# Kernel tuning notes

Hardware: AMD Instinct MI355X
Metric: run time of the kernel (lower is better)

## Reference

```python
import jax, jax.numpy as jnp
import numpy as np

B, S, D, H, L, V = 8, 512, 1024, 16, 12, 30145
FF = 4 * D
NL = 2  # n_langs
EPS = 1e-12


def _ln(x, g, b):
    m = jnp.mean(x, axis=-1, keepdims=True)
    v = jnp.var(x, axis=-1, keepdims=True)
    return (x - m) * jax.lax.rsqrt(v + EPS) * g + b


def setup_inputs() -> dict:
    key = jax.random.key(0)
    ks = iter(jax.random.split(key, 32))
    std, estd = 0.02, 0.02
    d = {
        "input_ids": jax.random.randint(next(ks), (B, S), 0, V),
        "langs": jax.random.randint(next(ks), (B, S), 0, NL),
        "attention_mask": jnp.ones((B, S), jnp.float32),
        "word_emb": jax.random.normal(next(ks), (V, D), jnp.float32) * estd,
        "pos_emb": jax.random.normal(next(ks), (S, D), jnp.float32) * estd,
        "lang_emb": jax.random.normal(next(ks), (NL, D), jnp.float32) * estd,
        "ln_emb_g": jnp.ones((D,), jnp.float32),
        "ln_emb_b": jnp.zeros((D,), jnp.float32),
        "Wq": jax.random.normal(next(ks), (L, D, D), jnp.float32) * std,
        "bq": jnp.zeros((L, D), jnp.float32),
        "Wk": jax.random.normal(next(ks), (L, D, D), jnp.float32) * std,
        "bk": jnp.zeros((L, D), jnp.float32),
        "Wv": jax.random.normal(next(ks), (L, D, D), jnp.float32) * std,
        "bv": jnp.zeros((L, D), jnp.float32),
        "Wo": jax.random.normal(next(ks), (L, D, D), jnp.float32) * std,
        "bo": jnp.zeros((L, D), jnp.float32),
        "ln1_g": jnp.ones((L, D), jnp.float32),
        "ln1_b": jnp.zeros((L, D), jnp.float32),
        "W1": jax.random.normal(next(ks), (L, D, FF), jnp.float32) * std,
        "b1": jnp.zeros((L, FF), jnp.float32),
        "W2": jax.random.normal(next(ks), (L, FF, D), jnp.float32) * std,
        "b2": jnp.zeros((L, D), jnp.float32),
        "ln2_g": jnp.ones((L, D), jnp.float32),
        "ln2_b": jnp.zeros((L, D), jnp.float32),
    }
    return d


def reference(input_ids, langs, attention_mask, word_emb, pos_emb, lang_emb,
              ln_emb_g, ln_emb_b, Wq, bq, Wk, bk, Wv, bv, Wo, bo,
              ln1_g, ln1_b, W1, b1, W2, b2, ln2_g, ln2_b):
    dh = D // H
    scale = 1.0 / np.sqrt(dh).astype(np.float32)
    # embeddings: word + position + language, then LayerNorm, then pad-mask
    x = word_emb[input_ids] + pos_emb[None, :, :] + lang_emb[langs]  # [B,S,D]
    x = _ln(x, ln_emb_g, ln_emb_b)
    fmask = attention_mask  # [B,S], 1=keep
    x = x * fmask[:, :, None]
    neg = (-1e30) * (1.0 - fmask)[:, None, None, :]  # [B,1,1,S] additive mask

    def layer(x, p):
        Wq_, bq_, Wk_, bk_, Wv_, bv_, Wo_, bo_, g1, gb1, W1_, b1_, W2_, b2_, g2, gb2 = p
        q = ((x @ Wq_ + bq_) * scale).reshape(B, S, H, dh)
        k = (x @ Wk_ + bk_).reshape(B, S, H, dh)
        v = (x @ Wv_ + bv_).reshape(B, S, H, dh)
        scores = jnp.einsum('bqhd,bkhd->bhqk', q, k) + neg
        w = jax.nn.softmax(scores, axis=-1)
        ctx = jnp.einsum('bhqk,bkhd->bqhd', w, v).reshape(B, S, D)
        x = _ln(x + ctx @ Wo_ + bo_, g1, gb1)
        h = jax.nn.gelu(x @ W1_ + b1_, approximate=False)  # erf gelu as in source
        x = _ln(x + h @ W2_ + b2_, g2, gb2)
        x = x * fmask[:, :, None]
        return x, None

    params = (Wq, bq, Wk, bk, Wv, bv, Wo, bo, ln1_g, ln1_b, W1, b1, W2, b2, ln2_g, ln2_b)
    x, _ = jax.lax.scan(layer, x, params)
    return x
```

## Files before the change

### kernel.cpp

```cpp
#include <hip/hip_runtime.h>
#include <math.h>

typedef float  f32x4  __attribute__((ext_vector_type(4)));
typedef __bf16 bf16x8 __attribute__((ext_vector_type(8)));
typedef __bf16 bf16x4 __attribute__((ext_vector_type(4)));

#define DEV __device__ __forceinline__

DEV f32x4 mfma16(bf16x8 a, bf16x8 b, f32x4 c) {
    return __builtin_amdgcn_mfma_f32_16x16x32_bf16(a, b, c, 0, 0, 0);
}

DEV void async16(const void* g, void* l) {
    __builtin_amdgcn_global_load_lds((const __attribute__((address_space(1))) void*)g,
                                     (__attribute__((address_space(3))) void*)l, 16, 0, 0);
}

constexpr int B_  = 8;
constexpr int S_  = 512;
constexpr int D_  = 1024;
constexpr int H_  = 16;
constexpr int FF_ = 4096;
constexpr int ROWS = B_ * S_;

__global__ __launch_bounds__(256)
void embed_ln_kernel(const int* __restrict__ ids, const int* __restrict__ lgs,
                     const float* __restrict__ fmask,
                     const float* __restrict__ wemb, const float* __restrict__ pemb,
                     const float* __restrict__ lemb,
                     const float* __restrict__ g, const float* __restrict__ bb,
                     float* __restrict__ xf, __bf16* __restrict__ xb)
{
    __shared__ float2 red[4];
    const int row = blockIdx.x;
    const int s   = row & (S_ - 1);
    const int t   = threadIdx.x;
    const int lane = t & 63, w = t >> 6;
    const int id = ids[row], lg = lgs[row];

    float4 wv = *(const float4*)(wemb + ((size_t)id << 10) + t * 4);
    float4 pv = *(const float4*)(pemb + ((size_t)s  << 10) + t * 4);
    float4 lv = *(const float4*)(lemb + ((size_t)lg << 10) + t * 4);
    float a[4] = { wv.x + pv.x + lv.x, wv.y + pv.y + lv.y,
                   wv.z + pv.z + lv.z, wv.w + pv.w + lv.w };

    float sm = a[0] + a[1] + a[2] + a[3];
    float sq = a[0]*a[0] + a[1]*a[1] + a[2]*a[2] + a[3]*a[3];
#pragma unroll
    for (int o = 32; o > 0; o >>= 1) { sm += __shfl_down(sm, o); sq += __shfl_down(sq, o); }
    if (lane == 0) red[w] = make_float2(sm, sq);
    __syncthreads();
    float ts = red[0].x + red[1].x + red[2].x + red[3].x;
    float tq = red[0].y + red[1].y + red[2].y + red[3].y;
    float mean = ts * (1.0f / D_);
    float var  = tq * (1.0f / D_) - mean * mean;
    float rs   = rsqrtf(var + 1e-12f);
    float fm   = fmask[row];

    float4 gv = *(const float4*)(g  + t * 4);
    float4 bv = *(const float4*)(bb + t * 4);
    float o0 = ((a[0]-mean)*rs*gv.x + bv.x) * fm;
    float o1 = ((a[1]-mean)*rs*gv.y + bv.y) * fm;
    float o2 = ((a[2]-mean)*rs*gv.z + bv.z) * fm;
    float o3 = ((a[3]-mean)*rs*gv.w + bv.w) * fm;
    *(float4*)(xf + ((size_t)row << 10) + t * 4) = make_float4(o0, o1, o2, o3);
    bf16x4 ob; ob[0] = (__bf16)o0; ob[1] = (__bf16)o1; ob[2] = (__bf16)o2; ob[3] = (__bf16)o3;
    *(bf16x4*)(xb + ((size_t)row << 10) + t * 4) = ob;
}

template<int NP>
__global__ __launch_bounds__(256)
void ln_resN_kernel(const float* __restrict__ xin, const float* __restrict__ y0,
                    const float* __restrict__ y1,
                    const float* __restrict__ g, const float* __restrict__ bb,
                    const float* __restrict__ fmask,
                    float* __restrict__ xf_out, __bf16* __restrict__ xb_out)
{
    constexpr size_t MN = (size_t)ROWS * D_;
    __shared__ float2 red[4];
    const int row = blockIdx.x;
    const int t   = threadIdx.x;
    const int lane = t & 63, w = t >> 6;
    const size_t base = ((size_t)row << 10) + t * 4;

    float4 xv = *(const float4*)(xin + base);
    float4 yv = *(const float4*)(y0 + base);
    float a[4] = { xv.x + yv.x, xv.y + yv.y, xv.z + yv.z, xv.w + yv.w };
    if (NP == 4) {
        float4 p1 = *(const float4*)(y0 + base + MN);
        float4 p2 = *(const float4*)(y1 + base);
        float4 p3 = *(const float4*)(y1 + base + MN);
        a[0] += p1.x + p2.x + p3.x; a[1] += p1.y + p2.y + p3.y;
        a[2] += p1.z + p2.z + p3.z; a[3] += p1.w + p2.w + p3.w;
    }

    float sm = a[0] + a[1] + a[2] + a[3];
    float sq = a[0]*a[0] + a[1]*a[1] + a[2]*a[2] + a[3]*a[3];
#pragma unroll
    for (int o = 32; o > 0; o >>= 1) { sm += __shfl_down(sm, o); sq += __shfl_down(sq, o); }
    if (lane == 0) red[w] = make_float2(sm, sq);
    __syncthreads();
    float ts = red[0].x + red[1].x + red[2].x + red[3].x;
    float tq = red[0].y + red[1].y + red[2].y + red[3].y;
    float mean = ts * (1.0f / D_);
    float var  = tq * (1.0f / D_) - mean * mean;
    float rs   = rsqrtf(var + 1e-12f);
    float fm   = fmask ? fmask[row] : 1.0f;

    float4 gv = *(const float4*)(g  + t * 4);
    float4 bv = *(const float4*)(bb + t * 4);
    float o0 = ((a[0]-mean)*rs*gv.x + bv.x) * fm;
    float o1 = ((a[1]-mean)*rs*gv.y + bv.y) * fm;
    float o2 = ((a[2]-mean)*rs*gv.z + bv.z) * fm;
    float o3 = ((a[3]-mean)*rs*gv.w + bv.w) * fm;
    *(float4*)(xf_out + base) = make_float4(o0, o1, o2, o3);
    bf16x4 ob; ob[0] = (__bf16)o0; ob[1] = (__bf16)o1; ob[2] = (__bf16)o2; ob[3] = (__bf16)o3;
    *(bf16x4*)(xb_out + base) = ob;
}

__global__ __launch_bounds__(256)
void conv_all_kernel(const float* __restrict__ Wq, const float* __restrict__ Wk,
                     const float* __restrict__ Wv, const float* __restrict__ Wo,
                     const float* __restrict__ W1, const float* __restrict__ W2,
                     __bf16* __restrict__ qkvT, __bf16* __restrict__ woT,
                     __bf16* __restrict__ w1T, __bf16* __restrict__ w2T)
{
    __shared__ __bf16 tile[64][66];
    const int id = blockIdx.x;
    const float* src; __bf16* dst; int K, N, t;
    if (id < 1024) {
        const int m = id >> 8; t = id & 255; K = 1024; N = 1024;
        src = (m == 0) ? Wq : (m == 1) ? Wk : (m == 2) ? Wv : Wo;
        dst = (m == 3) ? woT : qkvT + (size_t)m * 1024 * 1024;
    } else if (id < 2048) {
        t = id - 1024; K = 1024; N = 4096; src = W1; dst = w1T;
    } else {
        t = id - 2048; K = 4096; N = 1024; src = W2; dst = w2T;
    }
    const int ktiles = K >> 6;
    const int tk = t % ktiles, tn = t / ktiles;
    const int k0 = tk << 6, n0 = tn << 6;
    const int tt = threadIdx.x;
#pragma unroll
    for (int i = 0; i < 16; ++i) {
        int idx = i * 256 + tt;
        int r = idx >> 6, c = idx & 63;
        tile[c][r] = (__bf16)src[(size_t)(k0 + r) * N + n0 + c];
    }
    __syncthreads();
#pragma unroll
    for (int i = 0; i < 16; ++i) {
        int idx = i * 256 + tt;
        int r = idx >> 6, c = idx & 63;
        dst[(size_t)(n0 + r) * K + k0 + c] = tile[r][c];
    }
}

template<int EPI>
__global__ __launch_bounds__(512, 2)
void gemm256_kernel(const __bf16* __restrict__ A, const __bf16* __restrict__ Bt,
                    const float* __restrict__ b0, const float* __restrict__ b1,
                    const float* __restrict__ b2,
                    __bf16* __restrict__ o0, __bf16* __restrict__ o1,
                    __bf16* __restrict__ o2,
                    float* __restrict__ oF0, float* __restrict__ oF1,
                    int M, int N, int K, int Kloc, int nTn, int tiles)
{
    __shared__ __bf16 lds[65536];
    const int tid  = threadIdx.x;
    const int lane = tid & 63;
    const int w    = tid >> 6;
    const int wr   = w >> 2, wc = w & 3;

    const int nwg = gridDim.x, bid = blockIdx.x;
    const int cpx = nwg >> 3;
    const int bswz = (bid & 7) * cpx + (bid >> 3);
    const int slice = bswz / tiles;
    const int tile  = bswz % tiles;
    const int bm = tile / nTn, bn = tile % nTn;
    const int m0 = bm << 8, n0 = bn << 8;
    const int ks = slice * Kloc;

    const int rrT = tid >> 3;
    const size_t swzK  = (size_t)(((tid & 7) ^ (rrT & 7)) * 8);
    const size_t aoff0 = (size_t)rrT * K + swzK;
    const size_t boff0 = (size_t)((rrT >> 5) * 64 + (rrT & 31)) * K + swzK;
    const size_t boff1 = (size_t)(((rrT >> 5) + 2) * 64 + (rrT & 31)) * K + swzK;
    const int wub = w * 512;

    const int aread = (wr * 64 + (lane & 15)) * 64;
    const int bread = (wc * 32 + (lane & 15)) * 64;
    const int csw0 = ((      (lane >> 4) * 16) ^ ((lane & 7) << 4)) >> 1;
    const int csw1 = ((64 +  (lane >> 4) * 16) ^ ((lane & 7) << 4)) >> 1;

    f32x4 acc[8][4] = {};
    bf16x8 a_[4][2], b_[2][2];

#define ST_A(p,h,kt) do {                                                     \
    const size_t gb = (size_t)(m0 + (h) * 64) * K + (kt);                     \
    async16(A + gb + aoff0,                  lds + ((p)*2+(h))*8192 + wub);   \
    async16(A + gb + (size_t)128*K + aoff0,  lds + ((p)*2+(h))*8192 + 4096 + wub); \
} while (0)
#define ST_B(p,h,kt) do {                                                     \
    const size_t gb = (size_t)(n0 + (h) * 32) * K + (kt);                     \
    async16(Bt + gb + boff0, lds + 32768 + ((p)*2+(h))*8192 + wub);           \
    async16(Bt + gb + boff1, lds + 32768 + ((p)*2+(h))*8192 + 4096 + wub);    \
} while (0)
#define DS_A(p,h) do {                                                        \
    const __bf16* base_ = lds + ((p)*2+(h))*8192 + aread;                     \
    _Pragma("unroll") for (int m_ = 0; m_ < 4; ++m_) {                        \
        a_[m_][0] = *(const bf16x8*)(base_ + m_*1024 + csw0);                 \
        a_[m_][1] = *(const bf16x8*)(base_ + m_*1024 + csw1);                 \
    }                                                                         \
} while (0)
#define DS_B(p,h) do {                                                        \
    const __bf16* base_ = lds + 32768 + ((p)*2+(h))*8192 + bread;             \
    _Pragma("unroll") for (int n_ = 0; n_ < 2; ++n_) {                        \
        b_[n_][0] = *(const bf16x8*)(base_ + n_*1024 + csw0);                 \
        b_[n_][1] = *(const bf16x8*)(base_ + n_*1024 + csw1);                 \
    }                                                                         \
} while (0)
#define MM(mb,nb) do {                                                        \
    _Pragma("unroll") for (int m_ = 0; m_ < 4; ++m_)                          \
    _Pragma("unroll") for (int n_ = 0; n_ < 2; ++n_)                          \
    _Pragma("unroll") for (int k_ = 0; k_ < 2; ++k_)                          \
        acc[(mb)+m_][(nb)+n_] = mfma16(a_[m_][k_], b_[n_][k_], acc[(mb)+m_][(nb)+n_]); \
} while (0)
#define SYNC do { __builtin_amdgcn_s_barrier();                               \
    asm volatile("s_waitcnt lgkmcnt(0)" ::: "memory");                        \
    __builtin_amdgcn_s_setprio(1); } while (0)
#define PEND do { __builtin_amdgcn_s_setprio(0);                              \
    __builtin_amdgcn_s_barrier(); } while (0)

    ST_A(0,0, ks);      ST_B(0,1, ks);      ST_A(0,1, ks);      ST_B(0,0, ks);
    ST_A(1,0, ks + 64); ST_B(1,1, ks + 64); ST_A(1,1, ks + 64);
    asm volatile("s_waitcnt vmcnt(6)" ::: "memory");
    __builtin_amdgcn_s_barrier();

    const int nIter = Kloc >> 7;
    for (int i = 0; i < nIter; ++i) {
        const bool nl = (i != nIter - 1);
        const int kt1 = ks + (2*i+1) * 64;
        const int kt2 = ks + (2*i+2) * 64;
        const int kt3 = kt2 + 64;
        DS_A(0,0); DS_B(0,0); ST_B(1,0,kt1);
        SYNC; MM(0,0); PEND;
        DS_B(0,1); if (nl) ST_A(0,0,kt2);
        SYNC; MM(0,2); PEND;
        DS_A(0,1); if (nl) ST_B(0,1,kt2);
        SYNC; MM(4,2); PEND;
        DS_B(0,0); if (nl) ST_A(0,1,kt2);
        SYNC; MM(4,0);
        __builtin_amdgcn_s_setprio(0);
        if (nl) asm volatile("s_waitcnt vmcnt(6)" ::: "memory");
        else    asm volatile("s_waitcnt vmcnt(0)" ::: "memory");
        __builtin_amdgcn_s_barrier();
        DS_A(1,0); DS_B(1,0); if (nl) ST_B(0,0,kt2);
        SYNC; MM(0,0); PEND;
        DS_B(1,1); if (nl) ST_A(1,0,kt3);
        SYNC; MM(0,2); PEND;
        DS_A(1,1); if (nl) ST_B(1,1,kt3);
        SYNC; MM(4,2); PEND;
        DS_B(1,0); if (nl) ST_A(1,1,kt3);
        SYNC; MM(4,0);
        __builtin_amdgcn_s_setprio(0);
        if (nl) asm volatile("s_waitcnt vmcnt(6)" ::: "memory");
        __builtin_amdgcn_s_barrier();
    }
#undef ST_A
#undef ST_B
#undef DS_A
#undef DS_B
#undef MM
#undef SYNC
#undef PEND

    const int mrow = m0 + wr * 128 + (lane >> 4) * 4;
    const int ncol = n0 + wc * 64 + (lane & 15);
    if (EPI == 0) {
        const int sel = n0 >> 10;
        __bf16* out = (sel == 0) ? o0 : (sel == 1) ? o1 : o2;
        const float* bp = (sel == 0) ? b0 : (sel == 1) ? b1 : b2;
        const float scl = (sel == 0) ? 0.125f : 1.0f;
        const int nc = ncol & 1023;
#pragma unroll
        for (int ni = 0; ni < 4; ++ni) {
            const float bvv = bp[nc + ni * 16];
#pragma unroll
            for (int mi = 0; mi < 8; ++mi)
#pragma unroll
                for (int r = 0; r < 4; ++r)
                    out[(size_t)(mrow + mi * 16 + r) * D_ + nc + ni * 16] =
                        (__bf16)((acc[mi][ni][r] + bvv) * scl);
        }
    } else if (EPI == 2) {
#pragma unroll
        for (int ni = 0; ni < 4; ++ni) {
            const float bvv = b0[ncol + ni * 16];
#pragma unroll
            for (int mi = 0; mi < 8; ++mi)
#pragma unroll
                for (int r = 0; r < 4; ++r) {
                    float v = acc[mi][ni][r] + bvv;
                    float ge = 0.5f * v * (1.0f + erff(v * 0.70710678118654752f));
                    o0[(size_t)(mrow + mi * 16 + r) * N + ncol + ni * 16] = (__bf16)ge;
                }
        }
    } else {
        const size_t MN = (size_t)M * N;
        float* Y = (slice < 2) ? (oF0 + (size_t)slice * MN) : (oF1 + (size_t)(slice - 2) * MN);
#pragma unroll
        for (int ni = 0; ni < 4; ++ni) {
            const float bvv = (slice == 0) ? b0[ncol + ni * 16] : 0.0f;
#pragma unroll
            for (int mi = 0; mi < 8; ++mi)
#pragma unroll
                for (int r = 0; r < 4; ++r)
                    Y[(size_t)(mrow + mi * 16 + r) * N + ncol + ni * 16] = acc[mi][ni][r] + bvv;
        }
    }
}

template<int EPI>
__global__ __launch_bounds__(256, 2)
void gemm_kernel(const __bf16* __restrict__ A, const __bf16* __restrict__ Bt,
                 const float* __restrict__ bias, float* __restrict__ Cf,
                 __bf16* __restrict__ Cb, int M, int N, int K, float scale)
{
    __shared__ __bf16 As[128 * 64];
    __shared__ __bf16 Bs[128 * 64];
    const int tid = threadIdx.x;
    const int lane = tid & 63;
    const int w = tid >> 6, wr = w >> 1, wc = w & 1;
    const int nT = N >> 7;
    const int nwg = gridDim.x;
    const int bid = blockIdx.x;
    const int cpx = nwg >> 3;
    const int bswz = (bid & 7) * cpx + (bid >> 3);
    const int bm = bswz / nT, bn = bswz % nT;
    const int m0 = bm << 7, n0 = bn << 7;

    f32x4 acc[4][4] = {};

    const int chr = tid >> 3, chc = tid & 7;
    const __bf16* ga = A  + (size_t)(m0 + chr) * K + chc * 8;
    const __bf16* gb = Bt + (size_t)(n0 + chr) * K + chc * 8;
    char* la = (char*)As + (tid & ~63) * 16;
    char* lb = (char*)Bs + (tid & ~63) * 16;

    const __bf16* arow = As + (wr * 64 + (lane & 15)) * 64 + (lane >> 4) * 8;
    const __bf16* brow = Bs + (wc * 64 + (lane & 15)) * 64 + (lane >> 4) * 8;

    for (int k0 = 0; k0 < K; k0 += 64) {
#pragma unroll
        for (int i = 0; i < 4; ++i) {
            async16(ga + (size_t)(i * 32) * K + k0, la + i * 4096);
            async16(gb + (size_t)(i * 32) * K + k0, lb + i * 4096);
        }
        __syncthreads();
#pragma unroll
        for (int kk = 0; kk < 2; ++kk) {
            bf16x8 af[4], bf[4];
#pragma unroll
            for (int i = 0; i < 4; ++i) af[i] = *(const bf16x8*)(arow + i * 16 * 64 + kk * 32);
#pragma unroll
            for (int i = 0; i < 4; ++i) bf[i] = *(const bf16x8*)(brow + i * 16 * 64 + kk * 32);
#pragma unroll
            for (int mi = 0; mi < 4; ++mi)
#pragma unroll
                for (int ni = 0; ni < 4; ++ni)
                    acc[mi][ni] = mfma16(af[mi], bf[ni], acc[mi][ni]);
        }
        __syncthreads();
    }

    const int mb = m0 + wr * 64 + ((lane >> 4) * 4);
    const int nb = n0 + wc * 64 + (lane & 15);
#pragma unroll
    for (int ni = 0; ni < 4; ++ni) {
        const float bvv = bias[nb + ni * 16];
#pragma unroll
        for (int mi = 0; mi < 4; ++mi)
#pragma unroll
            for (int r = 0; r < 4; ++r)
                Cf[(size_t)(mb + mi * 16 + r) * N + nb + ni * 16] =
                    (acc[mi][ni][r] + bvv) * scale;
    }
}

__global__ __launch_bounds__(256, 2)
void attn_kernel(const __bf16* __restrict__ q, const __bf16* __restrict__ k,
                 const __bf16* __restrict__ v, const float* __restrict__ fmask,
                 __bf16* __restrict__ ctx)
{
    __shared__ __bf16 Ks[256 * 64];
    __shared__ __bf16 Vt[64 * 264];
    __shared__ float  negm[S_];
    const int bid = blockIdx.x;
    const int qt = bid & 7, h = (bid >> 3) & 15, b = bid >> 7;
    const int tid = threadIdx.x, lane = tid & 63, w = tid >> 6;
    const int r7 = lane & 7;

    const __bf16* kbase = k + ((size_t)b * S_) * D_ + h * 64;
    const __bf16* vbase = v + ((size_t)b * S_) * D_ + h * 64;
    char* kl = (char*)Ks + (tid & ~63) * 16;
    const int srow  = tid >> 3;
    const int sslot = (tid & 7) ^ (srow & 7);

    for (int i = tid; i < S_; i += 256) negm[i] = (fmask[b * S_ + i] - 1.0f) * 1e30f;

    const __bf16* qbase = q + ((size_t)b * S_ + qt * 64 + w * 16) * D_ + h * 64;
    const bf16x8 qf0 = *(const bf16x8*)(qbase + (size_t)(lane & 15) * D_ + (lane >> 4) * 8);
    const bf16x8 qf1 = *(const bf16x8*)(qbase + (size_t)(lane & 15) * D_ + 32 + (lane >> 4) * 8);

    f32x4 sc[32];
#pragma unroll
    for (int i = 0; i < 32; ++i) { sc[i][0] = 0.f; sc[i][1] = 0.f; sc[i][2] = 0.f; sc[i][3] = 0.f; }

#pragma unroll
    for (int c = 0; c < 2; ++c) {
        if (c) __syncthreads();
#pragma unroll
        for (int i = 0; i < 8; ++i) {
            const int s = c * 256 + i * 32 + srow;
            async16(kbase + (size_t)s * D_ + sslot * 8, kl + i * 4096);
        }
        __syncthreads();
#pragma unroll
        for (int nf = 0; nf < 16; ++nf) {
            const __bf16* kr = Ks + (nf * 16 + (lane & 15)) * 64;
            const bf16x8 k0 = *(const bf16x8*)(kr + ((((lane >> 4))     ^ r7) << 3));
            const bf16x8 k1 = *(const bf16x8*)(kr + ((((lane >> 4) + 4) ^ r7) << 3));
            sc[c * 16 + nf] = mfma16(qf0, k0, sc[c * 16 + nf]);
            sc[c * 16 + nf] = mfma16(qf1, k1, sc[c * 16 + nf]);
        }
    }

    float mx[4] = { -3e38f, -3e38f, -3e38f, -3e38f };
#pragma unroll
    for (int i = 0; i < 32; ++i) {
        const int key = (i >> 4) * 256 + (i & 15) * 16 + (lane & 15);
        const float nm = negm[key];
#pragma unroll
        for (int r = 0; r < 4; ++r) { sc[i][r] += nm; mx[r] = fmaxf(mx[r], sc[i][r]); }
    }
#pragma unroll
    for (int o = 8; o > 0; o >>= 1)
#pragma unroll
        for (int r = 0; r < 4; ++r) mx[r] = fmaxf(mx[r], __shfl_xor(mx[r], o));
    float smr[4] = { 0.f, 0.f, 0.f, 0.f };
#pragma unroll
    for (int i = 0; i < 32; ++i)
#pragma unroll
        for (int r = 0; r < 4; ++r) { float pp = __expf(sc[i][r] - mx[r]); sc[i][r] = pp; smr[r] += pp; }
#pragma unroll
    for (int o = 8; o > 0; o >>= 1)
#pragma unroll
        for (int r = 0; r < 4; ++r) smr[r] += __shfl_xor(smr[r], o);
    float inv[4];
#pragma unroll
    for (int r = 0; r < 4; ++r) inv[r] = 1.0f / smr[r];

    f32x4 co[4] = {};
#pragma unroll
    for (int c = 0; c < 2; ++c) {
        __syncthreads();
        __bf16* P = Ks + w * (16 * 256);
#pragma unroll
        for (int nf = 0; nf < 16; ++nf)
#pragma unroll
            for (int r = 0; r < 4; ++r) {
                const int row = (lane >> 4) * 4 + r;
                const int col = nf * 16 + (lane & 15);
                P[row * 256 + (((col >> 3) ^ (row & 7)) << 3) + (col & 7)] =
                    (__bf16)sc[c * 16 + nf][r];
            }
#pragma unroll
        for (int i = 0; i < 8; ++i) {
            const int s = i * 32 + (tid >> 3), d0 = (tid & 7) * 8;
            bf16x8 vv = *(const bf16x8*)(vbase + (size_t)(c * 256 + s) * D_ + d0);
#pragma unroll
            for (int j = 0; j < 8; ++j) Vt[(d0 + j) * 264 + s] = vv[j];
        }
        __syncthreads();
#pragma unroll
        for (int kk2 = 0; kk2 < 8; ++kk2) {
            const int row = lane & 15;
            const int slot = kk2 * 4 + (lane >> 4);
            bf16x8 pa = *(const bf16x8*)(P + row * 256 + ((slot ^ r7) << 3));
#pragma unroll
            for (int nf = 0; nf < 4; ++nf) {
                bf16x8 vf = *(const bf16x8*)(Vt + (nf * 16 + (lane & 15)) * 264 + kk2 * 32 + (lane >> 4) * 8);
                co[nf] = mfma16(pa, vf, co[nf]);
            }
        }
    }

    __bf16* cb = ctx + ((size_t)b * S_ + qt * 64 + w * 16) * D_ + h * 64;
#pragma unroll
    for (int nf = 0; nf < 4; ++nf)
#pragma unroll
        for (int r = 0; r < 4; ++r)
            cb[((lane >> 4) * 4 + r) * D_ + nf * 16 + (lane & 15)] = (__bf16)(co[nf][r] * inv[r]);
}

extern "C" void kernel_launch(void* const* d_in, const int* in_sizes, int n_in,
                              void* d_out, int out_size, void* d_ws, size_t ws_size,
                              hipStream_t stream)
{
    (void)in_sizes; (void)n_in; (void)out_size; (void)ws_size;
    const int*   ids   = (const int*)d_in[0];
    const int*   lgs   = (const int*)d_in[1];
    const float* amask = (const float*)d_in[2];
    const float* wemb  = (const float*)d_in[3];
    const float* pemb  = (const float*)d_in[4];
    const float* lemb  = (const float*)d_in[5];
    const float* lng   = (const float*)d_in[6];
    const float* lnbv  = (const float*)d_in[7];
    const float* Wq = (const float*)d_in[8];  const float* bq = (const float*)d_in[9];
    const float* Wk = (const float*)d_in[10]; const float* bk = (const float*)d_in[11];
    const float* Wv = (const float*)d_in[12]; const float* bv = (const float*)d_in[13];
    const float* Wo = (const float*)d_in[14]; const float* bo = (const float*)d_in[15];
    const float* g1 = (const float*)d_in[16]; const float* be1 = (const float*)d_in[17];
    const float* W1 = (const float*)d_in[18]; const float* b1 = (const float*)d_in[19];
    const float* W2 = (const float*)d_in[20]; const float* b2 = (const float*)d_in[21];
    const float* g2 = (const float*)d_in[22]; const float* be2 = (const float*)d_in[23];

    char* p = (char*)d_ws;
    auto take = [&](size_t n) { char* r = p; p += (n + 255) & ~(size_t)255; return r; };
    float*  xf    = (float*) take((size_t)ROWS * D_ * 4);
    __bf16* xb    = (__bf16*)take((size_t)ROWS * D_ * 2);
    __bf16* qb    = (__bf16*)take((size_t)ROWS * D_ * 2);
    __bf16* kb    = (__bf16*)take((size_t)ROWS * D_ * 2);
    __bf16* vbuf  = (__bf16*)take((size_t)ROWS * D_ * 2);
    __bf16* cxb   = (__bf16*)take((size_t)ROWS * D_ * 2);
    __bf16* hb    = (__bf16*)take((size_t)ROWS * FF_ * 2);
    float*  yfp   = (float*) take((size_t)2 * ROWS * D_ * 4);
    __bf16* wqkvT = (__bf16*)take((size_t)3 * D_ * D_ * 2);
    __bf16* woT   = (__bf16*)take((size_t)D_ * D_ * 2);
    __bf16* w1T   = (__bf16*)take((size_t)D_ * FF_ * 2);
    __bf16* w2T   = (__bf16*)take((size_t)FF_ * D_ * 2);
    float*  y23   = (float*)qb;

    const int gQKV = (ROWS / 256) * (3 * D_ / 256);
    const int gF1  = (ROWS / 256) * (FF_ / 256);
    const int gF2  = 4 * (ROWS / 256) * (D_ / 256);
    const int gWo  = (ROWS / 128) * (D_ / 128);

    embed_ln_kernel<<<ROWS, 256, 0, stream>>>(ids, lgs, amask, wemb, pemb, lemb, lng, lnbv, xf, xb);

    for (int l = 0; l < 12; ++l) {
        const size_t woff = (size_t)l * D_ * D_;
        const size_t foff = (size_t)l * D_ * FF_;
        conv_all_kernel<<<3072, 256, 0, stream>>>(Wq + woff, Wk + woff, Wv + woff, Wo + woff,
                                                  W1 + foff, W2 + foff,
                                                  wqkvT, woT, w1T, w2T);

        gemm256_kernel<0><<<gQKV, 512, 0, stream>>>(xb, wqkvT, bq + l * D_, bk + l * D_, bv + l * D_,
                                                    qb, kb, vbuf, nullptr, nullptr,
                                                    ROWS, 3 * D_, D_, D_, 12, gQKV);

        attn_kernel<<<B_ * H_ * (S_ / 64), 256, 0, stream>>>(qb, kb, vbuf, amask, cxb);

        gemm_kernel<1><<<gWo, 256, 0, stream>>>(cxb, woT, bo + l * D_, yfp, nullptr, ROWS, D_, D_, 1.0f);
        ln_resN_kernel<1><<<ROWS, 256, 0, stream>>>(xf, yfp, nullptr,
                                                    g1 + l * D_, be1 + l * D_, nullptr, xf, xb);

        gemm256_kernel<2><<<gF1, 512, 0, stream>>>(xb, w1T, b1 + l * FF_, nullptr, nullptr,
                                                   hb, nullptr, nullptr, nullptr, nullptr,
                                                   ROWS, FF_, D_, D_, 16, gF1);
        gemm256_kernel<3><<<gF2, 512, 0, stream>>>(hb, w2T, b2 + l * D_, nullptr, nullptr,
                                                   nullptr, nullptr, nullptr, yfp, y23,
                                                   ROWS, D_, FF_, D_, 4, 64);

        float* dst = (l == 11) ? (float*)d_out : xf;
        ln_resN_kernel<4><<<ROWS, 256, 0, stream>>>(xf, yfp, y23,
                                                    g2 + l * D_, be2 + l * D_, amask, dst, xb);
    }
}
```

Before: 2.724 ms.

## Store V transposed from QKV GEMM, bf16 partial sums, and restructure attention loads

```diff
diff --git a/kernel.cpp b/kernel.cpp
--- a/kernel.cpp
+++ b/kernel.cpp
@@ -70,8 +70,7 @@
 
 template<int NP>
 __global__ __launch_bounds__(256)
-void ln_resN_kernel(const float* __restrict__ xin, const float* __restrict__ y0,
-                    const float* __restrict__ y1,
+void ln_resN_kernel(const float* __restrict__ xin, const __bf16* __restrict__ yp,
                     const float* __restrict__ g, const float* __restrict__ bb,
                     const float* __restrict__ fmask,
                     float* __restrict__ xf_out, __bf16* __restrict__ xb_out)
@@ -84,14 +83,12 @@
     const size_t base = ((size_t)row << 10) + t * 4;
 
     float4 xv = *(const float4*)(xin + base);
-    float4 yv = *(const float4*)(y0 + base);
-    float a[4] = { xv.x + yv.x, xv.y + yv.y, xv.z + yv.z, xv.w + yv.w };
-    if (NP == 4) {
-        float4 p1 = *(const float4*)(y0 + base + MN);
-        float4 p2 = *(const float4*)(y1 + base);
-        float4 p3 = *(const float4*)(y1 + base + MN);
-        a[0] += p1.x + p2.x + p3.x; a[1] += p1.y + p2.y + p3.y;
-        a[2] += p1.z + p2.z + p3.z; a[3] += p1.w + p2.w + p3.w;
+    float a[4] = { xv.x, xv.y, xv.z, xv.w };
+#pragma unroll
+    for (int pslice = 0; pslice < NP; ++pslice) {
+        bf16x4 yv = *(const bf16x4*)(yp + base + (size_t)pslice * MN);
+#pragma unroll
+        for (int j = 0; j < 4; ++j) a[j] += (float)yv[j];
     }
 
     float sm = a[0] + a[1] + a[2] + a[3];
@@ -162,8 +159,7 @@
                     const float* __restrict__ b0, const float* __restrict__ b1,
                     const float* __restrict__ b2,
                     __bf16* __restrict__ o0, __bf16* __restrict__ o1,
-                    __bf16* __restrict__ o2,
-                    float* __restrict__ oF0, float* __restrict__ oF1,
+                    __bf16* __restrict__ o2, __bf16* __restrict__ oP,
                     int M, int N, int K, int Kloc, int nTn, int tiles)
 {
     __shared__ __bf16 lds[65536];
@@ -279,19 +275,37 @@
     const int ncol = n0 + wc * 64 + (lane & 15);
     if (EPI == 0) {
         const int sel = n0 >> 10;
-        __bf16* out = (sel == 0) ? o0 : (sel == 1) ? o1 : o2;
-        const float* bp = (sel == 0) ? b0 : (sel == 1) ? b1 : b2;
-        const float scl = (sel == 0) ? 0.125f : 1.0f;
         const int nc = ncol & 1023;
-#pragma unroll
-        for (int ni = 0; ni < 4; ++ni) {
-            const float bvv = bp[nc + ni * 16];
-#pragma unroll
-            for (int mi = 0; mi < 8; ++mi)
-#pragma unroll
-                for (int r = 0; r < 4; ++r)
-                    out[(size_t)(mrow + mi * 16 + r) * D_ + nc + ni * 16] =
-                        (__bf16)((acc[mi][ni][r] + bvv) * scl);
+        if (sel < 2) {
+            __bf16* out = (sel == 0) ? o0 : o1;
+            const float* bp = (sel == 0) ? b0 : b1;
+            const float scl = (sel == 0) ? 0.125f : 1.0f;
+#pragma unroll
+            for (int ni = 0; ni < 4; ++ni) {
+                const float bvv = bp[nc + ni * 16];
+#pragma unroll
+                for (int mi = 0; mi < 8; ++mi)
+#pragma unroll
+                    for (int r = 0; r < 4; ++r)
+                        out[(size_t)(mrow + mi * 16 + r) * D_ + nc + ni * 16] =
+                            (__bf16)((acc[mi][ni][r] + bvv) * scl);
+            }
+        } else {
+#pragma unroll
+            for (int ni = 0; ni < 4; ++ni) {
+                const int dhf = nc + ni * 16;
+                const float bvv = b2[dhf];
+                const int hh = dhf >> 6, dh = dhf & 63;
+#pragma unroll
+                for (int mi = 0; mi < 8; ++mi) {
+                    const int gm0 = mrow + mi * 16;
+                    const int bb_ = gm0 >> 9, s0 = gm0 & 511;
+                    bf16x4 pk;
+#pragma unroll
+                    for (int r = 0; r < 4; ++r) pk[r] = (__bf16)(acc[mi][ni][r] + bvv);
+                    *(bf16x4*)(o2 + ((size_t)((bb_ * 16 + hh) * 64 + dh) << 9) + s0) = pk;
+                }
+            }
         }
     } else if (EPI == 2) {
 #pragma unroll
@@ -307,8 +321,7 @@
                 }
         }
     } else {
-        const size_t MN = (size_t)M * N;
-        float* Y = (slice < 2) ? (oF0 + (size_t)slice * MN) : (oF1 + (size_t)(slice - 2) * MN);
+        __bf16* Y = oP + (size_t)slice * M * N;
 #pragma unroll
         for (int ni = 0; ni < 4; ++ni) {
             const float bvv = (slice == 0) ? b0[ncol + ni * 16] : 0.0f;
@@ -316,16 +329,16 @@
             for (int mi = 0; mi < 8; ++mi)
 #pragma unroll
                 for (int r = 0; r < 4; ++r)
-                    Y[(size_t)(mrow + mi * 16 + r) * N + ncol + ni * 16] = acc[mi][ni][r] + bvv;
+                    Y[(size_t)(mrow + mi * 16 + r) * N + ncol + ni * 16] =
+                        (__bf16)(acc[mi][ni][r] + bvv);
         }
     }
 }
 
-template<int EPI>
 __global__ __launch_bounds__(256, 2)
 void gemm_kernel(const __bf16* __restrict__ A, const __bf16* __restrict__ Bt,
-                 const float* __restrict__ bias, float* __restrict__ Cf,
-                 __bf16* __restrict__ Cb, int M, int N, int K, float scale)
+                 const float* __restrict__ bias, __bf16* __restrict__ Cb,
+                 int M, int N, int K)
 {
     __shared__ __bf16 As[128 * 64];
     __shared__ __bf16 Bs[128 * 64];
@@ -383,125 +396,119 @@
         for (int mi = 0; mi < 4; ++mi)
 #pragma unroll
             for (int r = 0; r < 4; ++r)
-                Cf[(size_t)(mb + mi * 16 + r) * N + nb + ni * 16] =
-                    (acc[mi][ni][r] + bvv) * scale;
+                Cb[(size_t)(mb + mi * 16 + r) * N + nb + ni * 16] =
+                    (__bf16)(acc[mi][ni][r] + bvv);
     }
 }
 
 __global__ __launch_bounds__(256, 2)
 void attn_kernel(const __bf16* __restrict__ q, const __bf16* __restrict__ k,
-                 const __bf16* __restrict__ v, const float* __restrict__ fmask,
+                 const __bf16* __restrict__ vT, const float* __restrict__ fmask,
                  __bf16* __restrict__ ctx)
 {
     __shared__ __bf16 Ks[256 * 64];
-    __shared__ __bf16 Vt[64 * 264];
+    __shared__ __bf16 Vt[64 * 256];
     __shared__ float  negm[S_];
     const int bid = blockIdx.x;
     const int qt = bid & 7, h = (bid >> 3) & 15, b = bid >> 7;
     const int tid = threadIdx.x, lane = tid & 63, w = tid >> 6;
-    const int r7 = lane & 7;
-
-    const __bf16* kbase = k + ((size_t)b * S_) * D_ + h * 64;
-    const __bf16* vbase = v + ((size_t)b * S_) * D_ + h * 64;
+    const int g = lane >> 4, q15 = lane & 15, r7 = lane & 7;
+
+    const __bf16* kbase  = k  + ((size_t)b * S_) * D_ + h * 64;
+    const __bf16* vTbase = vT + ((size_t)((b * 16 + h) * 64) << 9);
     char* kl = (char*)Ks + (tid & ~63) * 16;
+    char* vl = (char*)Vt + (tid & ~63) * 16;
     const int srow  = tid >> 3;
     const int sslot = (tid & 7) ^ (srow & 7);
-
+    const int vrow  = tid >> 5;
+#define ST_K(c) do { _Pragma("unroll") for (int i_ = 0; i_ < 8; ++i_) {       \
+        const int s_ = (c) * 256 + i_ * 32 + srow;                            \
+        async16(kbase + (size_t)s_ * D_ + sslot * 8, kl + i_ * 4096); } } while (0)
+#define ST_V(c) do { _Pragma("unroll") for (int i_ = 0; i_ < 8; ++i_) {       \
+        const int d_ = i_ * 8 + vrow;                                         \
+        async16(vTbase + ((size_t)d_ << 9) + (c) * 256 +                      \
+                (((tid & 31) ^ (d_ & 7)) << 3), vl + i_ * 4096); } } while (0)
+
+    ST_K(0);
     for (int i = tid; i < S_; i += 256) negm[i] = (fmask[b * S_ + i] - 1.0f) * 1e30f;
 
     const __bf16* qbase = q + ((size_t)b * S_ + qt * 64 + w * 16) * D_ + h * 64;
-    const bf16x8 qf0 = *(const bf16x8*)(qbase + (size_t)(lane & 15) * D_ + (lane >> 4) * 8);
-    const bf16x8 qf1 = *(const bf16x8*)(qbase + (size_t)(lane & 15) * D_ + 32 + (lane >> 4) * 8);
+    const bf16x8 qf0 = *(const bf16x8*)(qbase + (size_t)q15 * D_ + g * 8);
+    const bf16x8 qf1 = *(const bf16x8*)(qbase + (size_t)q15 * D_ + 32 + g * 8);
 
     f32x4 sc[32];
 #pragma unroll
     for (int i = 0; i < 32; ++i) { sc[i][0] = 0.f; sc[i][1] = 0.f; sc[i][2] = 0.f; sc[i][3] = 0.f; }
 
-#pragma unroll
-    for (int c = 0; c < 2; ++c) {
-        if (c) __syncthreads();
-#pragma unroll
-        for (int i = 0; i < 8; ++i) {
-            const int s = c * 256 + i * 32 + srow;
-            async16(kbase + (size_t)s * D_ + sslot * 8, kl + i * 4096);
-        }
-        __syncthreads();
-#pragma unroll
-        for (int nf = 0; nf < 16; ++nf) {
-            const __bf16* kr = Ks + (nf * 16 + (lane & 15)) * 64;
-            const bf16x8 k0 = *(const bf16x8*)(kr + ((((lane >> 4))     ^ r7) << 3));
-            const bf16x8 k1 = *(const bf16x8*)(kr + ((((lane >> 4) + 4) ^ r7) << 3));
-            sc[c * 16 + nf] = mfma16(qf0, k0, sc[c * 16 + nf]);
-            sc[c * 16 + nf] = mfma16(qf1, k1, sc[c * 16 + nf]);
-        }
-    }
-
-    float mx[4] = { -3e38f, -3e38f, -3e38f, -3e38f };
+#define QKT(c) do { _Pragma("unroll") for (int nf = 0; nf < 16; ++nf) {       \
+        const __bf16* kr = Ks + (nf * 16 + q15) * 64;                         \
+        const bf16x8 kf0 = *(const bf16x8*)(kr + ((g ^ r7) << 3));            \
+        const bf16x8 kf1 = *(const bf16x8*)(kr + (((g + 4) ^ r7) << 3));      \
+        sc[(c)*16+nf] = mfma16(kf0, qf0, sc[(c)*16+nf]);                      \
+        sc[(c)*16+nf] = mfma16(kf1, qf1, sc[(c)*16+nf]); } } while (0)
+
+    __syncthreads();
+    ST_V(0);
+    QKT(0);
+    __syncthreads();
+    ST_K(1);
+    __syncthreads();
+    QKT(1);
+
+    float mx = -3e38f;
 #pragma unroll
     for (int i = 0; i < 32; ++i) {
-        const int key = (i >> 4) * 256 + (i & 15) * 16 + (lane & 15);
-        const float nm = negm[key];
-#pragma unroll
-        for (int r = 0; r < 4; ++r) { sc[i][r] += nm; mx[r] = fmaxf(mx[r], sc[i][r]); }
-    }
-#pragma unroll
-    for (int o = 8; o > 0; o >>= 1)
-#pragma unroll
-        for (int r = 0; r < 4; ++r) mx[r] = fmaxf(mx[r], __shfl_xor(mx[r], o));
-    float smr[4] = { 0.f, 0.f, 0.f, 0.f };
+        const float4 nm4 = *(const float4*)(negm + ((i >> 4) * 256 + (i & 15) * 16 + 4 * g));
+        sc[i][0] += nm4.x; sc[i][1] += nm4.y; sc[i][2] += nm4.z; sc[i][3] += nm4.w;
+        mx = fmaxf(mx, fmaxf(fmaxf(sc[i][0], sc[i][1]), fmaxf(sc[i][2], sc[i][3])));
+    }
+    mx = fmaxf(mx, __shfl_xor(mx, 16));
+    mx = fmaxf(mx, __shfl_xor(mx, 32));
+    float sum = 0.f;
 #pragma unroll
     for (int i = 0; i < 32; ++i)
 #pragma unroll
-        for (int r = 0; r < 4; ++r) { float pp = __expf(sc[i][r] - mx[r]); sc[i][r] = pp; smr[r] += pp; }
-#pragma unroll
-    for (int o = 8; o > 0; o >>= 1)
-#pragma unroll
-        for (int r = 0; r < 4; ++r) smr[r] += __shfl_xor(smr[r], o);
-    float inv[4];
-#pragma unroll
-    for (int r = 0; r < 4; ++r) inv[r] = 1.0f / smr[r];
-
+        for (int r = 0; r < 4; ++r) { float pp = __expf(sc[i][r] - mx); sc[i][r] = pp; sum += pp; }
+    sum += __shfl_xor(sum, 16);
+    sum += __shfl_xor(sum, 32);
+    const float inv = 1.0f / sum;
+
+    __bf16* P = Ks + w * 4096;
     f32x4 co[4] = {};
-#pragma unroll
-    for (int c = 0; c < 2; ++c) {
-        __syncthreads();
-        __bf16* P = Ks + w * (16 * 256);
-#pragma unroll
-        for (int nf = 0; nf < 16; ++nf)
-#pragma unroll
-            for (int r = 0; r < 4; ++r) {
-                const int row = (lane >> 4) * 4 + r;
-                const int col = nf * 16 + (lane & 15);
-                P[row * 256 + (((col >> 3) ^ (row & 7)) << 3) + (col & 7)] =
-                    (__bf16)sc[c * 16 + nf][r];
-            }
-#pragma unroll
-        for (int i = 0; i < 8; ++i) {
-            const int s = i * 32 + (tid >> 3), d0 = (tid & 7) * 8;
-            bf16x8 vv = *(const bf16x8*)(vbase + (size_t)(c * 256 + s) * D_ + d0);
-#pragma unroll
-            for (int j = 0; j < 8; ++j) Vt[(d0 + j) * 264 + s] = vv[j];
-        }
-        __syncthreads();
-#pragma unroll
-        for (int kk2 = 0; kk2 < 8; ++kk2) {
-            const int row = lane & 15;
-            const int slot = kk2 * 4 + (lane >> 4);
-            bf16x8 pa = *(const bf16x8*)(P + row * 256 + ((slot ^ r7) << 3));
-#pragma unroll
-            for (int nf = 0; nf < 4; ++nf) {
-                bf16x8 vf = *(const bf16x8*)(Vt + (nf * 16 + (lane & 15)) * 264 + kk2 * 32 + (lane >> 4) * 8);
-                co[nf] = mfma16(pa, vf, co[nf]);
-            }
-        }
-    }
-
-    __bf16* cb = ctx + ((size_t)b * S_ + qt * 64 + w * 16) * D_ + h * 64;
-#pragma unroll
-    for (int nf = 0; nf < 4; ++nf)
-#pragma unroll
-        for (int r = 0; r < 4; ++r)
-            cb[((lane >> 4) * 4 + r) * D_ + nf * 16 + (lane & 15)] = (__bf16)(co[nf][r] * inv[r]);
+#define WR_P(c) do { _Pragma("unroll") for (int i_ = 0; i_ < 16; ++i_) {      \
+        bf16x4 pk;                                                            \
+        _Pragma("unroll") for (int r = 0; r < 4; ++r) pk[r] = (__bf16)sc[(c)*16+i_][r]; \
+        *(bf16x4*)(P + q15 * 256 + ((i_ * 16 + 4 * g) ^ (8 * r7))) = pk; } } while (0)
+#define PV() do { _Pragma("unroll") for (int kt = 0; kt < 8; ++kt) {          \
+        const bf16x8 pf = *(const bf16x8*)(P + q15 * 256 + ((kt * 32 + 8 * g) ^ (8 * r7))); \
+        _Pragma("unroll") for (int nf = 0; nf < 4; ++nf) {                    \
+            const int d_ = nf * 16 + q15;                                     \
+            const bf16x8 vf = *(const bf16x8*)(Vt + d_ * 256 + ((kt * 32 + 8 * g) ^ (8 * r7))); \
+            co[nf] = mfma16(vf, pf, co[nf]); } } } while (0)
+
+    __syncthreads();
+    WR_P(0);
+    __syncthreads();
+    PV();
+    __syncthreads();
+    WR_P(1);
+    ST_V(1);
+    __syncthreads();
+    PV();
+#undef ST_K
+#undef ST_V
+#undef QKT
+#undef WR_P
+#undef PV
+
+    __bf16* cb = ctx + ((size_t)b * S_ + qt * 64 + w * 16 + q15) * D_ + h * 64;
+#pragma unroll
+    for (int nf = 0; nf < 4; ++nf) {
+        bf16x4 o4;
+#pragma unroll
+        for (int r = 0; r < 4; ++r) o4[r] = (__bf16)(co[nf][r] * inv);
+        *(bf16x4*)(cb + nf * 16 + 4 * g) = o4;
+    }
 }
 
 extern "C" void kernel_launch(void* const* d_in, const int* in_sizes, int n_in,
@@ -532,15 +539,14 @@
     __bf16* xb    = (__bf16*)take((size_t)ROWS * D_ * 2);
     __bf16* qb    = (__bf16*)take((size_t)ROWS * D_ * 2);
     __bf16* kb    = (__bf16*)take((size_t)ROWS * D_ * 2);
-    __bf16* vbuf  = (__bf16*)take((size_t)ROWS * D_ * 2);
+    __bf16* vT    = (__bf16*)take((size_t)ROWS * D_ * 2);
     __bf16* cxb   = (__bf16*)take((size_t)ROWS * D_ * 2);
     __bf16* hb    = (__bf16*)take((size_t)ROWS * FF_ * 2);
-    float*  yfp   = (float*) take((size_t)2 * ROWS * D_ * 4);
+    __bf16* ybp   = (__bf16*)take((size_t)4 * ROWS * D_ * 2);
     __bf16* wqkvT = (__bf16*)take((size_t)3 * D_ * D_ * 2);
     __bf16* woT   = (__bf16*)take((size_t)D_ * D_ * 2);
     __bf16* w1T   = (__bf16*)take((size_t)D_ * FF_ * 2);
     __bf16* w2T   = (__bf16*)take((size_t)FF_ * D_ * 2);
-    float*  y23   = (float*)qb;
 
     const int gQKV = (ROWS / 256) * (3 * D_ / 256);
     const int gF1  = (ROWS / 256) * (FF_ / 256);
@@ -557,24 +563,24 @@
                                                   wqkvT, woT, w1T, w2T);
 
         gemm256_kernel<0><<<gQKV, 512, 0, stream>>>(xb, wqkvT, bq + l * D_, bk + l * D_, bv + l * D_,
-                                                    qb, kb, vbuf, nullptr, nullptr,
+                                                    qb, kb, vT, nullptr,
                                                     ROWS, 3 * D_, D_, D_, 12, gQKV);
 
-        attn_kernel<<<B_ * H_ * (S_ / 64), 256, 0, stream>>>(qb, kb, vbuf, amask, cxb);
-
-        gemm_kernel<1><<<gWo, 256, 0, stream>>>(cxb, woT, bo + l * D_, yfp, nullptr, ROWS, D_, D_, 1.0f);
-        ln_resN_kernel<1><<<ROWS, 256, 0, stream>>>(xf, yfp, nullptr,
-                                                    g1 + l * D_, be1 + l * D_, nullptr, xf, xb);
+        attn_kernel<<<B_ * H_ * (S_ / 64), 256, 0, stream>>>(qb, kb, vT, amask, cxb);
+
+        gemm_kernel<<<gWo, 256, 0, stream>>>(cxb, woT, bo + l * D_, ybp, ROWS, D_, D_);
+        ln_resN_kernel<1><<<ROWS, 256, 0, stream>>>(xf, ybp, g1 + l * D_, be1 + l * D_,
+                                                    nullptr, xf, xb);
 
         gemm256_kernel<2><<<gF1, 512, 0, stream>>>(xb, w1T, b1 + l * FF_, nullptr, nullptr,
-                                                   hb, nullptr, nullptr, nullptr, nullptr,
+                                                   hb, nullptr, nullptr, nullptr,
                                                    ROWS, FF_, D_, D_, 16, gF1);
         gemm256_kernel<3><<<gF2, 512, 0, stream>>>(hb, w2T, b2 + l * D_, nullptr, nullptr,
-                                                   nullptr, nullptr, nullptr, yfp, y23,
+                                                   nullptr, nullptr, nullptr, ybp,
                                                    ROWS, D_, FF_, D_, 4, 64);
 
         float* dst = (l == 11) ? (float*)d_out : xf;
-        ln_resN_kernel<4><<<ROWS, 256, 0, stream>>>(xf, yfp, y23,
-                                                    g2 + l * D_, be2 + l * D_, amask, dst, xb);
-    }
-}
+        ln_resN_kernel<4><<<ROWS, 256, 0, stream>>>(xf, ybp, g2 + l * D_, be2 + l * D_,
+                                                    amask, dst, xb);
+    }
+}
```

Measured after the change: 2.592 ms. 4.8% less time.
